# Kernel optimization log

Measured on AMD Instinct MI355X. Metric: run time of the kernel, lower is better.

## Reference

```python
import jax, jax.numpy as jnp
import numpy as np

N, F, DE = 768, 64, 32
H0, H1, H2, OUT = 64, 64, 128, 1  # hidden_dim=[64,64,128], output_dim=1


def _mlp(x, Wa, ba, Wb, bb):
    # two Dense layers with relu, as in the repo's MLP
    h = jax.nn.relu(x @ Wa + ba)
    return jax.nn.relu(h @ Wb + bb)


def _edge_conv_e(A, x, e, Wa, ba, Wb, bb):
    # EdgeConvE: per-edge message MLP([x_i, x_j - x_i, e_ij]) aggregated
    # over neighbors j weighted by the (binary) adjacency.
    n = x.shape[0]
    xi = jnp.broadcast_to(x[:, None, :], (n, n, x.shape[1]))  # [N,N,F]
    xj = jnp.broadcast_to(x[None, :, :], (n, n, x.shape[1]))  # [N,N,F]
    feat = jnp.concatenate([xi, xj - xi, e], axis=-1)         # [N,N,2F+De]
    m = _mlp(feat, Wa, ba, Wb, bb)                            # [N,N,H]
    return jnp.einsum('ij,ijh->ih', A, m)                     # scatter-sum over j


def setup_inputs() -> dict:
    key = jax.random.key(0)
    ks = jax.random.split(key, 16)
    adj = (jax.random.uniform(ks[0], (N, N)) < 0.05).astype(jnp.float32)
    x = jax.random.normal(ks[1], (N, F), dtype=jnp.float32)
    e = jax.random.normal(ks[2], (N, N, DE), dtype=jnp.float32)
    s = 0.05
    d_in1 = 2 * F + DE          # 160
    d_in2 = 2 * H0 + DE         # 160
    return {
        'ajacency': adj,
        'node_features': x,
        'edge_attributes': e,
        'W1a': jax.random.normal(ks[3], (d_in1, H0)) * s, 'b1a': jnp.zeros((H0,)),
        'W1b': jax.random.normal(ks[4], (H0, H0)) * s,    'b1b': jnp.zeros((H0,)),
        'W2a': jax.random.normal(ks[5], (d_in2, H1)) * s, 'b2a': jnp.zeros((H1,)),
        'W2b': jax.random.normal(ks[6], (H1, H0)) * s,    'b2b': jnp.zeros((H0,)),
        'W3': jax.random.normal(ks[7], (H0, H2)) * s,     'b3': jnp.zeros((H2,)),
        'W4': jax.random.normal(ks[8], (H2, OUT)) * s,    'b4': jnp.zeros((OUT,)),
    }


def reference(ajacency, node_features, edge_attributes,
              W1a, b1a, W1b, b1b, W2a, b2a, W2b, b2b, W3, b3, W4, b4):
    x = _edge_conv_e(ajacency, node_features, edge_attributes, W1a, b1a, W1b, b1b)
    x = _edge_conv_e(ajacency, x, edge_attributes, W2a, b2a, W2b, b2b)
    x = jax.nn.relu(x @ W3 + b3)
    return jax.nn.sigmoid(x @ W4 + b4)  # [N, OUT]
```

## Files before the change

### kernel.cpp

```cpp
#include <hip/hip_runtime.h>
#include <math.h>


#define NN 768
#define FF 64
#define DE 32
#define HH 64
#define CAP 128
#define SH1S 72

using bf16x8 = __attribute__((ext_vector_type(8))) short;
using f32x4  = __attribute__((ext_vector_type(4))) float;

__device__ __forceinline__ short f2b(float f) {
  unsigned u = __float_as_uint(f);
  return (short)((u + 0x7fffu + ((u >> 16) & 1u)) >> 16);
}

__global__ __launch_bounds__(256) void scan_kernel(
    const float* __restrict__ A, const float* __restrict__ x,
    const float* __restrict__ e,
    const float* __restrict__ W, const float* __restrict__ bias,
    const float* __restrict__ We1, const float* __restrict__ We2,
    const float* __restrict__ Wb1, const float* __restrict__ Wb2,
    int* __restrict__ cnt, int* __restrict__ jl,
    float* __restrict__ U, float* __restrict__ V,
    float* __restrict__ ew1, float* __restrict__ ew2,
    short* __restrict__ Wbp1, short* __restrict__ Wbp2)
{
  const int i = blockIdx.x;
  const int tid = threadIdx.x;
  __shared__ int s_cnt;
  __shared__ int s_j[CAP];
  __shared__ float sx[64];
  __shared__ float su[4][64], sv[4][64];
  __shared__ __align__(16) float es[CAP][DE];

  if (tid == 0) s_cnt = 0;
  __syncthreads();
  if (tid < 64) sx[tid] = x[i * 64 + tid];
  if (tid < NN / 4) {
    float4 a = ((const float4*)(A + i * NN))[tid];
    if (a.x != 0.0f) { int p = atomicAdd(&s_cnt, 1); if (p < CAP) s_j[p] = tid * 4 + 0; }
    if (a.y != 0.0f) { int p = atomicAdd(&s_cnt, 1); if (p < CAP) s_j[p] = tid * 4 + 1; }
    if (a.z != 0.0f) { int p = atomicAdd(&s_cnt, 1); if (p < CAP) s_j[p] = tid * 4 + 2; }
    if (a.w != 0.0f) { int p = atomicAdd(&s_cnt, 1); if (p < CAP) s_j[p] = tid * 4 + 3; }
  }
  __syncthreads();
  const int c = min(s_cnt, CAP);

  for (int slot = tid >> 3; slot < c; slot += 32) {
    const int j = s_j[slot];
    ((float4*)es[slot])[tid & 7] =
        ((const float4*)(e + ((size_t)i * NN + j) * DE))[tid & 7];
  }

  const int c64 = tid & 63, sg = tid >> 6;
  float w1[DE], w2[DE];
#pragma unroll
  for (int d = 0; d < DE; ++d) { w1[d] = We1[d * HH + c64]; w2[d] = We2[d * HH + c64]; }
  __syncthreads();

  for (int slot = sg; slot < c; slot += 4) {
    float a1 = 0.0f, a2 = 0.0f;
#pragma unroll
    for (int d = 0; d < DE; ++d) {
      const float f = es[slot][d];
      a1 = fmaf(f, w1[d], a1);
      a2 = fmaf(f, w2[d], a2);
    }
    ew1[((size_t)(i << 7) + slot) * HH + c64] = a1;
    ew2[((size_t)(i << 7) + slot) * HH + c64] = a2;
  }

  {
    float u = 0.0f, v = 0.0f;
#pragma unroll
    for (int t = 0; t < 16; ++t) {
      const int d = sg * 16 + t;
      const float xv = sx[d];
      const float wxi = W[d * 64 + c64];
      const float wxj = W[(64 + d) * 64 + c64];
      u = fmaf(xv, wxi - wxj, u);
      v = fmaf(xv, wxj, v);
    }
    su[sg][c64] = u; sv[sg][c64] = v;
  }

  if (i < 2) {
    const float* src = (i == 0) ? Wb1 : Wb2;
    short* dst = (i == 0) ? Wbp1 : Wbp2;
    for (int L = tid; L < 4096; L += 256) {
      const int j = L & 7, n = (L >> 3) & 15, quad = (L >> 7) & 3;
      const int kb = (L >> 9) & 1, ct = L >> 10;
      dst[L] = f2b(src[(kb * 32 + quad * 8 + j) * 64 + ct * 16 + n]);
    }
  }
  __syncthreads();

  if (tid < 64) {
    U[i * 64 + tid] = su[0][tid] + su[1][tid] + su[2][tid] + su[3][tid] + bias[tid];
    V[i * 64 + tid] = sv[0][tid] + sv[1][tid] + sv[2][tid] + sv[3][tid];
  }
  if (tid == 0) cnt[i] = c;
  for (int t = tid; t < c; t += 256) jl[(i << 7) + t] = s_j[t];
}

__device__ __forceinline__ void conv_body(
    int i, int c, const int* __restrict__ jl,
    const float* __restrict__ U, const float* __restrict__ V,
    const float* __restrict__ ew, const short* __restrict__ Wbp,
    const float* __restrict__ bb, short* sh1b, float* xrow,
    int tid, int lane, int wv)
{
  const int nt = (c + 15) >> 4;
  const int cpad = nt << 4;

  if (c > 0) {
    const float u_i = U[(i << 6) + lane];
    for (int slot = wv; slot < cpad; slot += 4) {
      short val = 0;
      if (slot < c) {
        const int j = jl[(i << 7) + slot];
        const float h = u_i + V[(j << 6) + lane]
                      + ew[((size_t)(i << 7) + slot) * HH + lane];
        val = f2b(fmaxf(h, 0.0f));
      }
      sh1b[slot * SH1S + lane] = val;
    }
  }
  __syncthreads();

  if (c > 0) {
    const int q = lane >> 4, n = lane & 15;
    bf16x8 b0 = *(const bf16x8*)(Wbp + (((wv * 2 + 0) * 4 + q) * 16 + n) * 8);
    bf16x8 b1 = *(const bf16x8*)(Wbp + (((wv * 2 + 1) * 4 + q) * 16 + n) * 8);
    const float bias = bb[wv * 16 + n];
    float s = 0.0f;
    for (int rt = 0; rt < nt; ++rt) {
      const short* sa = sh1b + (rt * 16 + n) * SH1S + q * 8;
      bf16x8 a0 = *(const bf16x8*)(sa);
      bf16x8 a1 = *(const bf16x8*)(sa + 32);
      f32x4 acc = {0.f, 0.f, 0.f, 0.f};
      acc = __builtin_amdgcn_mfma_f32_16x16x32_bf16(a0, b0, acc, 0, 0, 0);
      acc = __builtin_amdgcn_mfma_f32_16x16x32_bf16(a1, b1, acc, 0, 0, 0);
#pragma unroll
      for (int reg = 0; reg < 4; ++reg) {
        const int row = rt * 16 + q * 4 + reg;
        const float v = fmaxf(acc[reg] + bias, 0.0f);
        s += (row < c) ? v : 0.0f;
      }
    }
    s += __shfl_down(s, 32);
    s += __shfl_down(s, 16);
    if (lane < 16) xrow[wv * 16 + lane] = s;
  } else {
    if (lane < 16) xrow[wv * 16 + lane] = 0.0f;
  }
  __syncthreads();
}

__global__ __launch_bounds__(256) void conv1uv2_kernel(
    const int* __restrict__ cnt, const int* __restrict__ jl,
    const float* __restrict__ U1, const float* __restrict__ V1,
    const float* __restrict__ ew1, const short* __restrict__ Wbp1,
    const float* __restrict__ b1b,
    const float* __restrict__ W2a, const float* __restrict__ b2a,
    float* __restrict__ U2, float* __restrict__ V2)
{
  const int i = blockIdx.x;
  const int tid = threadIdx.x, lane = tid & 63, wv = tid >> 6;
  __shared__ __align__(16) short sh1b[CAP * SH1S];
  __shared__ float xrow[64];
  __shared__ float su[4][64], sv[4][64];

  conv_body(i, cnt[i], jl, U1, V1, ew1, Wbp1, b1b, sh1b, xrow, tid, lane, wv);

  const int c64 = tid & 63, qr = tid >> 6;
  {
    float u = 0.0f, v = 0.0f;
#pragma unroll
    for (int t = 0; t < 16; ++t) {
      const int d = qr * 16 + t;
      const float xv = xrow[d];
      const float wxi = W2a[d * 64 + c64];
      const float wxj = W2a[(64 + d) * 64 + c64];
      u = fmaf(xv, wxi - wxj, u);
      v = fmaf(xv, wxj, v);
    }
    su[qr][c64] = u; sv[qr][c64] = v;
  }
  __syncthreads();
  if (tid < 64) {
    U2[i * 64 + tid] = su[0][tid] + su[1][tid] + su[2][tid] + su[3][tid] + b2a[tid];
    V2[i * 64 + tid] = sv[0][tid] + sv[1][tid] + sv[2][tid] + sv[3][tid];
  }
}

__global__ __launch_bounds__(256) void conv2head_kernel(
    const int* __restrict__ cnt, const int* __restrict__ jl,
    const float* __restrict__ U2, const float* __restrict__ V2,
    const float* __restrict__ ew2, const short* __restrict__ Wbp2,
    const float* __restrict__ b2b,
    const float* __restrict__ W3, const float* __restrict__ b3,
    const float* __restrict__ W4, const float* __restrict__ b4,
    float* __restrict__ out)
{
  const int i = blockIdx.x;
  const int tid = threadIdx.x, lane = tid & 63, wv = tid >> 6;
  __shared__ __align__(16) short sh1b[CAP * SH1S];
  __shared__ float xrow[64];
  __shared__ float sred[2];

  conv_body(i, cnt[i], jl, U2, V2, ew2, Wbp2, b2b, sh1b, xrow, tid, lane, wv);

  if (tid < 128) {
    float p = b3[tid];
#pragma unroll
    for (int c = 0; c < 64; ++c) p = fmaf(xrow[c], W3[c * 128 + tid], p);
    p = fmaxf(p, 0.0f);
    float v = p * W4[tid];
    v += __shfl_down(v, 32);
    v += __shfl_down(v, 16);
    v += __shfl_down(v, 8);
    v += __shfl_down(v, 4);
    v += __shfl_down(v, 2);
    v += __shfl_down(v, 1);
    if (lane == 0) sred[wv] = v;
  }
  __syncthreads();
  if (tid == 0) {
    const float z = sred[0] + sred[1] + b4[0];
    out[i] = 1.0f / (1.0f + expf(-z));
  }
}

extern "C" void kernel_launch(void* const* d_in, const int* in_sizes, int n_in,
                              void* d_out, int out_size, void* d_ws, size_t ws_size,
                              hipStream_t stream) {
  const float* A   = (const float*)d_in[0];
  const float* x   = (const float*)d_in[1];
  const float* e   = (const float*)d_in[2];
  const float* W1a = (const float*)d_in[3];
  const float* b1a = (const float*)d_in[4];
  const float* W1b = (const float*)d_in[5];
  const float* b1b = (const float*)d_in[6];
  const float* W2a = (const float*)d_in[7];
  const float* b2a = (const float*)d_in[8];
  const float* W2b = (const float*)d_in[9];
  const float* b2b = (const float*)d_in[10];
  const float* W3  = (const float*)d_in[11];
  const float* b3  = (const float*)d_in[12];
  const float* W4  = (const float*)d_in[13];
  const float* b4  = (const float*)d_in[14];
  float* out = (float*)d_out;

  int*   cnt  = (int*)d_ws;
  int*   jl   = cnt + NN;
  float* U1   = (float*)(jl + NN * CAP);
  float* V1   = U1 + NN * HH;
  float* U2   = V1 + NN * HH;
  float* V2   = U2 + NN * HH;
  float* ew1  = V2 + NN * HH;
  float* ew2  = ew1 + (size_t)NN * CAP * HH;
  short* Wbp1 = (short*)(ew2 + (size_t)NN * CAP * HH);
  short* Wbp2 = Wbp1 + 4096;

  scan_kernel<<<NN, 256, 0, stream>>>(A, x, e, W1a, b1a,
                                      W1a + 128 * HH, W2a + 128 * HH,
                                      W1b, W2b,
                                      cnt, jl, U1, V1, ew1, ew2, Wbp1, Wbp2);
  conv1uv2_kernel<<<NN, 256, 0, stream>>>(cnt, jl, U1, V1, ew1, Wbp1, b1b,
                                          W2a, b2a, U2, V2);
  conv2head_kernel<<<NN, 256, 0, stream>>>(cnt, jl, U2, V2, ew2, Wbp2, b2b,
                                           W3, b3, W4, b4, out);
}
```

Baseline: 163.2 us.

## Fuse edge-attribute projection into conv1 and store layer-2 edge term as bf16

The per-edge projection e_ij·We moves out of the scan kernel and into the first conv kernel, where it is computed inline while building the hidden activations. This removes the fp32 ew1 round trip through global memory. The layer-2 edge term is still precomputed, but it is written in bf16, halving that intermediate's traffic. In exchange the conv1 kernel uses more shared memory and registers, and the layer-2 edge term loses some precision.

```diff
diff --git a/kernel.cpp b/kernel.cpp
--- a/kernel.cpp
+++ b/kernel.cpp
@@ -16,122 +16,16 @@
   unsigned u = __float_as_uint(f);
   return (short)((u + 0x7fffu + ((u >> 16) & 1u)) >> 16);
 }
-
-__global__ __launch_bounds__(256) void scan_kernel(
-    const float* __restrict__ A, const float* __restrict__ x,
-    const float* __restrict__ e,
-    const float* __restrict__ W, const float* __restrict__ bias,
-    const float* __restrict__ We1, const float* __restrict__ We2,
-    const float* __restrict__ Wb1, const float* __restrict__ Wb2,
-    int* __restrict__ cnt, int* __restrict__ jl,
-    float* __restrict__ U, float* __restrict__ V,
-    float* __restrict__ ew1, float* __restrict__ ew2,
-    short* __restrict__ Wbp1, short* __restrict__ Wbp2)
-{
-  const int i = blockIdx.x;
-  const int tid = threadIdx.x;
-  __shared__ int s_cnt;
-  __shared__ int s_j[CAP];
-  __shared__ float sx[64];
-  __shared__ float su[4][64], sv[4][64];
-  __shared__ __align__(16) float es[CAP][DE];
-
-  if (tid == 0) s_cnt = 0;
-  __syncthreads();
-  if (tid < 64) sx[tid] = x[i * 64 + tid];
-  if (tid < NN / 4) {
-    float4 a = ((const float4*)(A + i * NN))[tid];
-    if (a.x != 0.0f) { int p = atomicAdd(&s_cnt, 1); if (p < CAP) s_j[p] = tid * 4 + 0; }
-    if (a.y != 0.0f) { int p = atomicAdd(&s_cnt, 1); if (p < CAP) s_j[p] = tid * 4 + 1; }
-    if (a.z != 0.0f) { int p = atomicAdd(&s_cnt, 1); if (p < CAP) s_j[p] = tid * 4 + 2; }
-    if (a.w != 0.0f) { int p = atomicAdd(&s_cnt, 1); if (p < CAP) s_j[p] = tid * 4 + 3; }
-  }
-  __syncthreads();
-  const int c = min(s_cnt, CAP);
-
-  for (int slot = tid >> 3; slot < c; slot += 32) {
-    const int j = s_j[slot];
-    ((float4*)es[slot])[tid & 7] =
-        ((const float4*)(e + ((size_t)i * NN + j) * DE))[tid & 7];
-  }
-
-  const int c64 = tid & 63, sg = tid >> 6;
-  float w1[DE], w2[DE];
-#pragma unroll
-  for (int d = 0; d < DE; ++d) { w1[d] = We1[d * HH + c64]; w2[d] = We2[d * HH + c64]; }
-  __syncthreads();
-
-  for (int slot = sg; slot < c; slot += 4) {
-    float a1 = 0.0f, a2 = 0.0f;
-#pragma unroll
-    for (int d = 0; d < DE; ++d) {
-      const float f = es[slot][d];
-      a1 = fmaf(f, w1[d], a1);
-      a2 = fmaf(f, w2[d], a2);
-    }
-    ew1[((size_t)(i << 7) + slot) * HH + c64] = a1;
-    ew2[((size_t)(i << 7) + slot) * HH + c64] = a2;
-  }
-
-  {
-    float u = 0.0f, v = 0.0f;
-#pragma unroll
-    for (int t = 0; t < 16; ++t) {
-      const int d = sg * 16 + t;
-      const float xv = sx[d];
-      const float wxi = W[d * 64 + c64];
-      const float wxj = W[(64 + d) * 64 + c64];
-      u = fmaf(xv, wxi - wxj, u);
-      v = fmaf(xv, wxj, v);
-    }
-    su[sg][c64] = u; sv[sg][c64] = v;
-  }
-
-  if (i < 2) {
-    const float* src = (i == 0) ? Wb1 : Wb2;
-    short* dst = (i == 0) ? Wbp1 : Wbp2;
-    for (int L = tid; L < 4096; L += 256) {
-      const int j = L & 7, n = (L >> 3) & 15, quad = (L >> 7) & 3;
-      const int kb = (L >> 9) & 1, ct = L >> 10;
-      dst[L] = f2b(src[(kb * 32 + quad * 8 + j) * 64 + ct * 16 + n]);
-    }
-  }
-  __syncthreads();
-
-  if (tid < 64) {
-    U[i * 64 + tid] = su[0][tid] + su[1][tid] + su[2][tid] + su[3][tid] + bias[tid];
-    V[i * 64 + tid] = sv[0][tid] + sv[1][tid] + sv[2][tid] + sv[3][tid];
-  }
-  if (tid == 0) cnt[i] = c;
-  for (int t = tid; t < c; t += 256) jl[(i << 7) + t] = s_j[t];
-}
-
-__device__ __forceinline__ void conv_body(
-    int i, int c, const int* __restrict__ jl,
-    const float* __restrict__ U, const float* __restrict__ V,
-    const float* __restrict__ ew, const short* __restrict__ Wbp,
-    const float* __restrict__ bb, short* sh1b, float* xrow,
-    int tid, int lane, int wv)
-{
-  const int nt = (c + 15) >> 4;
-  const int cpad = nt << 4;
-
+__device__ __forceinline__ float b2f(unsigned short u) {
+  return __uint_as_float(((unsigned)u) << 16);
+}
+
+__device__ __forceinline__ void phaseB(
+    const short* sh1b, const short* __restrict__ Wbp,
+    const float* __restrict__ bb, float* xrow, int c, int lane, int wv)
+{
   if (c > 0) {
-    const float u_i = U[(i << 6) + lane];
-    for (int slot = wv; slot < cpad; slot += 4) {
-      short val = 0;
-      if (slot < c) {
-        const int j = jl[(i << 7) + slot];
-        const float h = u_i + V[(j << 6) + lane]
-                      + ew[((size_t)(i << 7) + slot) * HH + lane];
-        val = f2b(fmaxf(h, 0.0f));
-      }
-      sh1b[slot * SH1S + lane] = val;
-    }
-  }
-  __syncthreads();
-
-  if (c > 0) {
+    const int nt = (c + 15) >> 4;
     const int q = lane >> 4, n = lane & 15;
     bf16x8 b0 = *(const bf16x8*)(Wbp + (((wv * 2 + 0) * 4 + q) * 16 + n) * 8);
     bf16x8 b1 = *(const bf16x8*)(Wbp + (((wv * 2 + 1) * 4 + q) * 16 + n) * 8);
@@ -157,24 +51,128 @@
   } else {
     if (lane < 16) xrow[wv * 16 + lane] = 0.0f;
   }
-  __syncthreads();
+}
+
+__global__ __launch_bounds__(256) void scan_kernel(
+    const float* __restrict__ A, const float* __restrict__ x,
+    const float* __restrict__ W, const float* __restrict__ bias,
+    const float* __restrict__ Wb1, const float* __restrict__ Wb2,
+    int* __restrict__ cnt, int* __restrict__ jl,
+    float* __restrict__ U, float* __restrict__ V,
+    short* __restrict__ Wbp1, short* __restrict__ Wbp2)
+{
+  const int i = blockIdx.x;
+  const int tid = threadIdx.x;
+  __shared__ int s_cnt;
+  __shared__ int s_j[CAP];
+  __shared__ float sx[64];
+  __shared__ float su[4][64], sv[4][64];
+
+  if (tid == 0) s_cnt = 0;
+  __syncthreads();
+  if (tid < 64) sx[tid] = x[i * 64 + tid];
+  if (tid < NN / 4) {
+    float4 a = ((const float4*)(A + i * NN))[tid];
+    if (a.x != 0.0f) { int p = atomicAdd(&s_cnt, 1); if (p < CAP) s_j[p] = tid * 4 + 0; }
+    if (a.y != 0.0f) { int p = atomicAdd(&s_cnt, 1); if (p < CAP) s_j[p] = tid * 4 + 1; }
+    if (a.z != 0.0f) { int p = atomicAdd(&s_cnt, 1); if (p < CAP) s_j[p] = tid * 4 + 2; }
+    if (a.w != 0.0f) { int p = atomicAdd(&s_cnt, 1); if (p < CAP) s_j[p] = tid * 4 + 3; }
+  }
+
+  if (i < 2) {
+    const float* src = (i == 0) ? Wb1 : Wb2;
+    short* dst = (i == 0) ? Wbp1 : Wbp2;
+    for (int L = tid; L < 4096; L += 256) {
+      const int j = L & 7, n = (L >> 3) & 15, quad = (L >> 7) & 3;
+      const int kb = (L >> 9) & 1, ct = L >> 10;
+      dst[L] = f2b(src[(kb * 32 + quad * 8 + j) * 64 + ct * 16 + n]);
+    }
+  }
+  __syncthreads();
+  const int c = min(s_cnt, CAP);
+
+  const int c64 = tid & 63, sg = tid >> 6;
+  {
+    float u = 0.0f, v = 0.0f;
+#pragma unroll
+    for (int t = 0; t < 16; ++t) {
+      const int d = sg * 16 + t;
+      const float xv = sx[d];
+      const float wxi = W[d * 64 + c64];
+      const float wxj = W[(64 + d) * 64 + c64];
+      u = fmaf(xv, wxi - wxj, u);
+      v = fmaf(xv, wxj, v);
+    }
+    su[sg][c64] = u; sv[sg][c64] = v;
+  }
+  __syncthreads();
+
+  if (tid < 64) {
+    U[i * 64 + tid] = su[0][tid] + su[1][tid] + su[2][tid] + su[3][tid] + bias[tid];
+    V[i * 64 + tid] = sv[0][tid] + sv[1][tid] + sv[2][tid] + sv[3][tid];
+  }
+  if (tid == 0) cnt[i] = c;
+  for (int t = tid; t < c; t += 256) jl[(i << 7) + t] = s_j[t];
 }
 
 __global__ __launch_bounds__(256) void conv1uv2_kernel(
     const int* __restrict__ cnt, const int* __restrict__ jl,
+    const float* __restrict__ e,
     const float* __restrict__ U1, const float* __restrict__ V1,
-    const float* __restrict__ ew1, const short* __restrict__ Wbp1,
-    const float* __restrict__ b1b,
+    const float* __restrict__ We1, const float* __restrict__ We2,
+    const short* __restrict__ Wbp1, const float* __restrict__ b1b,
     const float* __restrict__ W2a, const float* __restrict__ b2a,
-    float* __restrict__ U2, float* __restrict__ V2)
+    float* __restrict__ U2, float* __restrict__ V2,
+    unsigned short* __restrict__ ew2b)
 {
   const int i = blockIdx.x;
   const int tid = threadIdx.x, lane = tid & 63, wv = tid >> 6;
+  __shared__ __align__(16) float es[CAP][DE];
   __shared__ __align__(16) short sh1b[CAP * SH1S];
+  __shared__ int s_j[CAP];
   __shared__ float xrow[64];
   __shared__ float su[4][64], sv[4][64];
 
-  conv_body(i, cnt[i], jl, U1, V1, ew1, Wbp1, b1b, sh1b, xrow, tid, lane, wv);
+  const int c = cnt[i];
+  for (int t = tid; t < c; t += 256) s_j[t] = jl[(i << 7) + t];
+  __syncthreads();
+
+  for (int slot = tid >> 3; slot < c; slot += 32) {
+    const int j = s_j[slot];
+    ((float4*)es[slot])[tid & 7] =
+        ((const float4*)(e + ((size_t)i * NN + j) * DE))[tid & 7];
+  }
+
+  float w1e[DE], w2e[DE];
+#pragma unroll
+  for (int d = 0; d < DE; ++d) { w1e[d] = We1[d * HH + lane]; w2e[d] = We2[d * HH + lane]; }
+  __syncthreads();
+
+  if (c > 0) {
+    const int cpad = ((c + 15) >> 4) << 4;
+    const float u_i = U1[(i << 6) + lane];
+    for (int slot = wv; slot < cpad; slot += 4) {
+      short val = 0;
+      if (slot < c) {
+        const int j = s_j[slot];
+        float h = u_i + V1[(j << 6) + lane];
+        float g = 0.0f;
+#pragma unroll
+        for (int d = 0; d < DE; ++d) {
+          const float f = es[slot][d];
+          h = fmaf(f, w1e[d], h);
+          g = fmaf(f, w2e[d], g);
+        }
+        val = f2b(fmaxf(h, 0.0f));
+        ew2b[((size_t)(i << 7) + slot) * HH + lane] = (unsigned short)f2b(g);
+      }
+      sh1b[slot * SH1S + lane] = val;
+    }
+  }
+  __syncthreads();
+
+  phaseB(sh1b, Wbp1, b1b, xrow, c, lane, wv);
+  __syncthreads();
 
   const int c64 = tid & 63, qr = tid >> 6;
   {
@@ -200,7 +198,7 @@
 __global__ __launch_bounds__(256) void conv2head_kernel(
     const int* __restrict__ cnt, const int* __restrict__ jl,
     const float* __restrict__ U2, const float* __restrict__ V2,
-    const float* __restrict__ ew2, const short* __restrict__ Wbp2,
+    const unsigned short* __restrict__ ew2b, const short* __restrict__ Wbp2,
     const float* __restrict__ b2b,
     const float* __restrict__ W3, const float* __restrict__ b3,
     const float* __restrict__ W4, const float* __restrict__ b4,
@@ -212,12 +210,30 @@
   __shared__ float xrow[64];
   __shared__ float sred[2];
 
-  conv_body(i, cnt[i], jl, U2, V2, ew2, Wbp2, b2b, sh1b, xrow, tid, lane, wv);
+  const int c = cnt[i];
+  if (c > 0) {
+    const int cpad = ((c + 15) >> 4) << 4;
+    const float u_i = U2[(i << 6) + lane];
+    for (int slot = wv; slot < cpad; slot += 4) {
+      short val = 0;
+      if (slot < c) {
+        const int j = jl[(i << 7) + slot];
+        const float h = u_i + V2[(j << 6) + lane]
+                      + b2f(ew2b[((size_t)(i << 7) + slot) * HH + lane]);
+        val = f2b(fmaxf(h, 0.0f));
+      }
+      sh1b[slot * SH1S + lane] = val;
+    }
+  }
+  __syncthreads();
+
+  phaseB(sh1b, Wbp2, b2b, xrow, c, lane, wv);
+  __syncthreads();
 
   if (tid < 128) {
     float p = b3[tid];
 #pragma unroll
-    for (int c = 0; c < 64; ++c) p = fmaf(xrow[c], W3[c * 128 + tid], p);
+    for (int cc = 0; cc < 64; ++cc) p = fmaf(xrow[cc], W3[cc * 128 + tid], p);
     p = fmaxf(p, 0.0f);
     float v = p * W4[tid];
     v += __shfl_down(v, 32);
@@ -261,17 +277,15 @@
   float* V1   = U1 + NN * HH;
   float* U2   = V1 + NN * HH;
   float* V2   = U2 + NN * HH;
-  float* ew1  = V2 + NN * HH;
-  float* ew2  = ew1 + (size_t)NN * CAP * HH;
-  short* Wbp1 = (short*)(ew2 + (size_t)NN * CAP * HH);
+  unsigned short* ew2b = (unsigned short*)(V2 + NN * HH);
+  short* Wbp1 = (short*)(ew2b + (size_t)NN * CAP * HH);
   short* Wbp2 = Wbp1 + 4096;
 
-  scan_kernel<<<NN, 256, 0, stream>>>(A, x, e, W1a, b1a,
-                                      W1a + 128 * HH, W2a + 128 * HH,
-                                      W1b, W2b,
-                                      cnt, jl, U1, V1, ew1, ew2, Wbp1, Wbp2);
-  conv1uv2_kernel<<<NN, 256, 0, stream>>>(cnt, jl, U1, V1, ew1, Wbp1, b1b,
-                                          W2a, b2a, U2, V2);
-  conv2head_kernel<<<NN, 256, 0, stream>>>(cnt, jl, U2, V2, ew2, Wbp2, b2b,
+  scan_kernel<<<NN, 256, 0, stream>>>(A, x, W1a, b1a, W1b, W2b,
+                                      cnt, jl, U1, V1, Wbp1, Wbp2);
+  conv1uv2_kernel<<<NN, 256, 0, stream>>>(cnt, jl, e, U1, V1,
+                                          W1a + 128 * HH, W2a + 128 * HH,
+                                          Wbp1, b1b, W2a, b2a, U2, V2, ew2b);
+  conv2head_kernel<<<NN, 256, 0, stream>>>(cnt, jl, U2, V2, ew2b, Wbp2, b2b,
                                            W3, b3, W4, b4, out);
 }
```

Result: faster. 153.0 us (-6.2%).
